# Kernel tuning notes

Measured on AMD Instinct MI355X. Metric: run time of the kernel, lower is better.

## Reference

```python
import jax, jax.numpy as jnp
import numpy as np

BITS = 2
ALPHA = 1.47


def lecac_quantize(w, bits=BITS, alpha=ALPHA):
    """2-bit alpha-scaled weight quantization (LECAC-style fake quant).

    Per-tensor scale derived from mean |w|, scaled by alpha. For bits=2 the
    integer codes live in [-2, 1] (i.e. [-2^(b-1), 2^(b-1)-1]).
    Straight-through estimator: gradient flows as identity through the
    round/clip (stop_gradient trick).
    """
    qmin = -(2 ** (bits - 1))          # -2
    qmax = 2 ** (bits - 1) - 1         # +1
    scale = alpha * jnp.mean(jnp.abs(w)) + jnp.asarray(1e-8, w.dtype)
    q = jnp.clip(jnp.round(w / scale), qmin, qmax)
    w_q = scale * q
    # STE: forward uses w_q, backward passes grad straight through to w
    return w + jax.lax.stop_gradient(w_q - w)


def lecac_linear(x, w, b):
    return jnp.dot(x, lecac_quantize(w).T) + b


def setup_inputs() -> dict:
    key = jax.random.key(0)
    kx, kw1, kb1, kw2, kb2 = jax.random.split(key, 5)
    B, D_IN, D_HID = 262144, 256, 512
    x = jax.random.normal(kx, (B, D_IN), dtype=jnp.float32)
    # Kaiming-ish init like nn.Linear
    W1 = jax.random.normal(kw1, (D_HID, D_IN), dtype=jnp.float32) * (1.0 / np.sqrt(D_IN))
    b1 = jax.random.normal(kb1, (D_HID,), dtype=jnp.float32) * 0.01
    W2 = jax.random.normal(kw2, (D_IN, D_HID), dtype=jnp.float32) * (1.0 / np.sqrt(D_HID))
    b2 = jax.random.normal(kb2, (D_IN,), dtype=jnp.float32) * 0.01
    return {"x": x, "W1": W1, "b1": b1, "W2": W2, "b2": b2}


def reference(x, W1, b1, W2, b2):
    h = jax.nn.relu(lecac_linear(x, W1, b1))   # [B, 512]
    return lecac_linear(h, W2, b2)             # [B, 256]
```

## Files before the change

### kernel.cpp

```cpp
#include <hip/hip_runtime.h>
#include <hip/hip_bf16.h>


typedef __attribute__((ext_vector_type(8))) short bf16x8;
typedef __attribute__((ext_vector_type(4))) float f32x4;
typedef __attribute__((ext_vector_type(4))) unsigned short us4;

#define D_IN 256
#define D_HID 512
#define D_OUT 256
#define BM 32

__device__ __forceinline__ unsigned short f2bf(float f) {
  union { __hip_bfloat16 h; unsigned short u; } c;
  c.h = __float2bfloat16(f);
  return c.u;
}

__device__ __forceinline__ bf16x8 cvt8(float4 lo, float4 hi) {
  bf16x8 v;
  v[0] = (short)f2bf(lo.x); v[1] = (short)f2bf(lo.y);
  v[2] = (short)f2bf(lo.z); v[3] = (short)f2bf(lo.w);
  v[4] = (short)f2bf(hi.x); v[5] = (short)f2bf(hi.y);
  v[6] = (short)f2bf(hi.z); v[7] = (short)f2bf(hi.w);
  return v;
}

__device__ __forceinline__ bf16x8 unpack8(unsigned w, int kkl) {
  unsigned te = (w >> (4 * kkl)) & 0x03030303u;
  unsigned to = (w >> (4 * kkl + 2)) & 0x03030303u;
  int4 o;
  unsigned s;
  s = __builtin_amdgcn_perm(to, te, 0x04040000u) + 0x00040004u;
  o.x = (int)__builtin_amdgcn_perm(0x80008000u, 0xBFC03F00u, s);
  s = __builtin_amdgcn_perm(to, te, 0x05050101u) + 0x00040004u;
  o.y = (int)__builtin_amdgcn_perm(0x80008000u, 0xBFC03F00u, s);
  s = __builtin_amdgcn_perm(to, te, 0x06060202u) + 0x00040004u;
  o.z = (int)__builtin_amdgcn_perm(0x80008000u, 0xBFC03F00u, s);
  s = __builtin_amdgcn_perm(to, te, 0x07070303u) + 0x00040004u;
  o.w = (int)__builtin_amdgcn_perm(0x80008000u, 0xBFC03F00u, s);
  return *(bf16x8*)&o;
}

__global__ void partial_abs_kernel(const float* __restrict__ W1,
                                   const float* __restrict__ W2,
                                   double* __restrict__ part) {
  const int b = blockIdx.x;
  const float* W = (b < 8) ? W1 : W2;
  const float* p = W + (b & 7) * 16384;
  double s = 0.0;
  for (int i = threadIdx.x; i < 16384; i += 1024) s += (double)fabsf(p[i]);
  __shared__ double red[1024];
  red[threadIdx.x] = s;
  __syncthreads();
  for (int st = 512; st > 0; st >>= 1) {
    if (threadIdx.x < st) red[threadIdx.x] += red[threadIdx.x + st];
    __syncthreads();
  }
  if (threadIdx.x == 0) part[b] = red[0];
}

__global__ void pack_kernel(const float* __restrict__ W1,
                            const float* __restrict__ W2,
                            const double* __restrict__ part,
                            unsigned* __restrict__ pk,
                            float* __restrict__ fscales) {
  int idx = blockIdx.x * 1024 + threadIdx.x;
  const double* q = part;
  double sA = 1.47 * ((((q[0]+q[1])+(q[2]+q[3]))+((q[4]+q[5])+(q[6]+q[7]))) / 131072.0) + 1e-8;
  double sB = 1.47 * ((((q[8]+q[9])+(q[10]+q[11]))+((q[12]+q[13])+(q[14]+q[15]))) / 131072.0) + 1e-8;
  if (idx == 0) { fscales[0] = (float)sA; fscales[1] = (float)sB; }
  bool is2 = idx >= 8192;
  int r = idx & 8191;
  int tt = r >> 4;
  int w = r & 15;
  int wv = tt >> 6, lane = tt & 63;
  int l15 = lane & 15, g = (lane >> 4) & 3;
  unsigned word = 0;
  for (int c = 0; c < 4; ++c) {
    for (int b = 0; b < 4; ++b) {
      int j = 2 * b + (c & 1), kkl = c >> 1;
      int code;
      if (!is2) {
        int mf = w >> 2, kp = w & 3;
        int row = 64 * wv + 16 * mf + l15;
        int k = (2 * kp + kkl) * 32 + 8 * g + j;
        double v = rint((double)W1[row * 256 + k] / sA);
        code = (int)fmin(fmax(v, -2.0), 1.0) & 3;
      } else {
        int mf = w >> 3, kp = w & 7;
        int row = 32 * wv + 16 * mf + l15;
        int k = (2 * kp + kkl) * 32 + 8 * g + j;
        double v = rint((double)W2[row * 512 + k] / sB);
        code = (int)fmin(fmax(v, -2.0), 1.0) & 3;
      }
      word |= (unsigned)code << (8 * b + 2 * c);
    }
  }
  pk[idx] = word;
}

__launch_bounds__(512)
__global__ void fused_mlp(const float* __restrict__ x,
                          const float* __restrict__ b1,
                          const float* __restrict__ b2,
                          const unsigned* __restrict__ pk,
                          const float* __restrict__ fscales,
                          float* __restrict__ out) {
  __shared__ unsigned short xs[BM * D_IN];
  __shared__ unsigned short hs[BM * D_HID];
  const int t = threadIdx.x;
  const int lane = t & 63;
  const int wv = t >> 6;
  const int l15 = lane & 15;
  const int g = lane >> 4;
  const long row0 = (long)blockIdx.x * BM;
  const float s1 = fscales[0];
  const float s2 = fscales[1];
  const f32x4 zero4 = {0.f, 0.f, 0.f, 0.f};

  unsigned w1k[16], w2k[16];
  {
    const uint4* p1 = (const uint4*)pk + t * 4;
    const uint4* p2 = (const uint4*)pk + 2048 + t * 4;
#pragma unroll
    for (int i = 0; i < 4; ++i) {
      uint4 a = p1[i], b = p2[i];
      w1k[4*i] = a.x; w1k[4*i+1] = a.y; w1k[4*i+2] = a.z; w1k[4*i+3] = a.w;
      w2k[4*i] = b.x; w2k[4*i+1] = b.y; w2k[4*i+2] = b.z; w2k[4*i+3] = b.w;
    }
  }

  {
    const float4* p = (const float4*)x + (long)blockIdx.x * 2048 + (t >> 4) * 64 + (t & 15) * 4;
    float4 v0 = p[0], v1 = p[1], v2 = p[2], v3 = p[3];
    int r = t >> 4, cq = t & 15;
    bf16x8 e0 = cvt8(v0, v1);
    bf16x8 e1 = cvt8(v2, v3);
    int sw = (r & 7) << 2;
    *(bf16x8*)&xs[r * 256 + ((cq * 2) ^ sw) * 8] = e0;
    *(bf16x8*)&xs[r * 256 + ((cq * 2 + 1) ^ sw) * 8] = e1;
  }
  __syncthreads();

  f32x4 acc1[4][2];
#pragma unroll
  for (int a = 0; a < 4; ++a) { acc1[a][0] = zero4; acc1[a][1] = zero4; }
#pragma unroll
  for (int kp = 0; kp < 4; ++kp) {
#pragma unroll
    for (int kkl = 0; kkl < 2; ++kkl) {
      int kk = 2 * kp + kkl;
      bf16x8 bx[2];
#pragma unroll
      for (int nf = 0; nf < 2; ++nf) {
        int m = 16 * nf + l15;
        int s = (kk * 4 + g) ^ ((m & 7) << 2);
        bx[nf] = *(const bf16x8*)&xs[m * 256 + s * 8];
      }
#pragma unroll
      for (int mf = 0; mf < 4; ++mf) {
        bf16x8 fr = unpack8(w1k[mf * 4 + kp], kkl);
        acc1[mf][0] = __builtin_amdgcn_mfma_f32_16x16x32_bf16(fr, bx[0], acc1[mf][0], 0, 0, 0);
        acc1[mf][1] = __builtin_amdgcn_mfma_f32_16x16x32_bf16(fr, bx[1], acc1[mf][1], 0, 0, 0);
      }
    }
  }

#pragma unroll
  for (int mf = 0; mf < 4; ++mf) {
    int cb = 64 * wv + 16 * mf + 4 * g;
    float4 bb = *(const float4*)&b1[cb];
    int chunk = 8 * wv + 2 * mf + (g >> 1);
    int half = (g & 1) * 4;
#pragma unroll
    for (int nf = 0; nf < 2; ++nf) {
      int m = 16 * nf + l15;
      f32x4 a = acc1[mf][nf];
      us4 o;
      o.x = f2bf(fmaxf(s1 * a[0] + bb.x, 0.f));
      o.y = f2bf(fmaxf(s1 * a[1] + bb.y, 0.f));
      o.z = f2bf(fmaxf(s1 * a[2] + bb.z, 0.f));
      o.w = f2bf(fmaxf(s1 * a[3] + bb.w, 0.f));
      int slot = chunk ^ ((m & 7) << 2);
      *(us4*)&hs[m * D_HID + slot * 8 + half] = o;
    }
  }
  __syncthreads();

  f32x4 acc2[2][2];
#pragma unroll
  for (int a = 0; a < 2; ++a) { acc2[a][0] = zero4; acc2[a][1] = zero4; }
#pragma unroll
  for (int kp = 0; kp < 8; ++kp) {
#pragma unroll
    for (int kkl = 0; kkl < 2; ++kkl) {
      int kk = 2 * kp + kkl;
      bf16x8 bh[2];
#pragma unroll
      for (int nf = 0; nf < 2; ++nf) {
        int m = 16 * nf + l15;
        int s = (kk * 4 + g) ^ ((m & 7) << 2);
        bh[nf] = *(const bf16x8*)&hs[m * D_HID + s * 8];
      }
#pragma unroll
      for (int mf = 0; mf < 2; ++mf) {
        bf16x8 fr = unpack8(w2k[mf * 8 + kp], kkl);
        acc2[mf][0] = __builtin_amdgcn_mfma_f32_16x16x32_bf16(fr, bh[0], acc2[mf][0], 0, 0, 0);
        acc2[mf][1] = __builtin_amdgcn_mfma_f32_16x16x32_bf16(fr, bh[1], acc2[mf][1], 0, 0, 0);
      }
    }
  }

#pragma unroll
  for (int mf = 0; mf < 2; ++mf) {
    int n4 = 32 * wv + 16 * mf + 4 * g;
    float4 bb = *(const float4*)&b2[n4];
#pragma unroll
    for (int nf = 0; nf < 2; ++nf) {
      int m = 16 * nf + l15;
      f32x4 a = acc2[mf][nf];
      float4 o;
      o.x = s2 * a[0] + bb.x;
      o.y = s2 * a[1] + bb.y;
      o.z = s2 * a[2] + bb.z;
      o.w = s2 * a[3] + bb.w;
      *(float4*)&out[(row0 + m) * D_OUT + n4] = o;
    }
  }
}

extern "C" void kernel_launch(void* const* d_in, const int* in_sizes, int n_in,
                              void* d_out, int out_size, void* d_ws, size_t ws_size,
                              hipStream_t stream) {
  const float* x  = (const float*)d_in[0];
  const float* W1 = (const float*)d_in[1];
  const float* b1 = (const float*)d_in[2];
  const float* W2 = (const float*)d_in[3];
  const float* b2 = (const float*)d_in[4];
  float* out = (float*)d_out;

  double* part = (double*)d_ws;
  float* fsc = (float*)((char*)d_ws + 128);
  unsigned* pk = (unsigned*)((char*)d_ws + 1024);

  int Brows = in_sizes[0] / D_IN;
  int nblk = Brows / BM;

  partial_abs_kernel<<<dim3(16), dim3(1024), 0, stream>>>(W1, W2, part);
  pack_kernel<<<dim3(16), dim3(1024), 0, stream>>>(W1, W2, part, pk, fsc);
  fused_mlp<<<dim3(nblk), dim3(512), 0, stream>>>(x, b1, b2, pk, fsc, out);
}
```

Before: 220.1 us.

## Persistent 1024-thread blocks over 4 row tiles with double-buffered x prefetch

```diff
diff --git a/kernel.cpp b/kernel.cpp
--- a/kernel.cpp
+++ b/kernel.cpp
@@ -9,7 +9,8 @@
 #define D_IN 256
 #define D_HID 512
 #define D_OUT 256
-#define BM 32
+#define BM 64
+#define TILES 4
 
 __device__ __forceinline__ unsigned short f2bf(float f) {
   union { __hip_bfloat16 h; unsigned short u; } c;
@@ -72,8 +73,8 @@
   if (idx == 0) { fscales[0] = (float)sA; fscales[1] = (float)sB; }
   bool is2 = idx >= 8192;
   int r = idx & 8191;
-  int tt = r >> 4;
-  int w = r & 15;
+  int tt = r >> 3;
+  int w = r & 7;
   int wv = tt >> 6, lane = tt & 63;
   int l15 = lane & 15, g = (lane >> 4) & 3;
   unsigned word = 0;
@@ -83,13 +84,13 @@
       int code;
       if (!is2) {
         int mf = w >> 2, kp = w & 3;
-        int row = 64 * wv + 16 * mf + l15;
+        int row = 32 * wv + 16 * mf + l15;
         int k = (2 * kp + kkl) * 32 + 8 * g + j;
         double v = rint((double)W1[row * 256 + k] / sA);
         code = (int)fmin(fmax(v, -2.0), 1.0) & 3;
       } else {
-        int mf = w >> 3, kp = w & 7;
-        int row = 32 * wv + 16 * mf + l15;
+        int kp = w;
+        int row = 16 * wv + l15;
         int k = (2 * kp + kkl) * 32 + 8 * g + j;
         double v = rint((double)W2[row * 512 + k] / sB);
         code = (int)fmin(fmax(v, -2.0), 1.0) & 3;
@@ -100,133 +101,157 @@
   pk[idx] = word;
 }
 
-__launch_bounds__(512)
+__launch_bounds__(1024)
 __global__ void fused_mlp(const float* __restrict__ x,
                           const float* __restrict__ b1,
                           const float* __restrict__ b2,
                           const unsigned* __restrict__ pk,
                           const float* __restrict__ fscales,
                           float* __restrict__ out) {
-  __shared__ unsigned short xs[BM * D_IN];
+  __shared__ unsigned short xs[2][BM * D_IN];
   __shared__ unsigned short hs[BM * D_HID];
   const int t = threadIdx.x;
   const int lane = t & 63;
   const int wv = t >> 6;
   const int l15 = lane & 15;
   const int g = lane >> 4;
-  const long row0 = (long)blockIdx.x * BM;
+  const long tbase = (long)blockIdx.x * TILES;
   const float s1 = fscales[0];
   const float s2 = fscales[1];
   const f32x4 zero4 = {0.f, 0.f, 0.f, 0.f};
 
-  unsigned w1k[16], w2k[16];
+  unsigned w1k[8], w2k[8];
   {
-    const uint4* p1 = (const uint4*)pk + t * 4;
-    const uint4* p2 = (const uint4*)pk + 2048 + t * 4;
-#pragma unroll
-    for (int i = 0; i < 4; ++i) {
+    const uint4* p1 = (const uint4*)pk + t * 2;
+    const uint4* p2 = (const uint4*)(pk + 8192) + t * 2;
+#pragma unroll
+    for (int i = 0; i < 2; ++i) {
       uint4 a = p1[i], b = p2[i];
       w1k[4*i] = a.x; w1k[4*i+1] = a.y; w1k[4*i+2] = a.z; w1k[4*i+3] = a.w;
       w2k[4*i] = b.x; w2k[4*i+1] = b.y; w2k[4*i+2] = b.z; w2k[4*i+3] = b.w;
     }
   }
 
-  {
-    const float4* p = (const float4*)x + (long)blockIdx.x * 2048 + (t >> 4) * 64 + (t & 15) * 4;
-    float4 v0 = p[0], v1 = p[1], v2 = p[2], v3 = p[3];
-    int r = t >> 4, cq = t & 15;
-    bf16x8 e0 = cvt8(v0, v1);
-    bf16x8 e1 = cvt8(v2, v3);
-    int sw = (r & 7) << 2;
-    *(bf16x8*)&xs[r * 256 + ((cq * 2) ^ sw) * 8] = e0;
-    *(bf16x8*)&xs[r * 256 + ((cq * 2 + 1) ^ sw) * 8] = e1;
-  }
-  __syncthreads();
-
-  f32x4 acc1[4][2];
-#pragma unroll
-  for (int a = 0; a < 4; ++a) { acc1[a][0] = zero4; acc1[a][1] = zero4; }
-#pragma unroll
-  for (int kp = 0; kp < 4; ++kp) {
-#pragma unroll
-    for (int kkl = 0; kkl < 2; ++kkl) {
-      int kk = 2 * kp + kkl;
-      bf16x8 bx[2];
-#pragma unroll
-      for (int nf = 0; nf < 2; ++nf) {
+  float4 xv[4];
+
+  auto loadxv = [&](long tile) {
+    const float4* p = (const float4*)x + tile * 4096;
+    xv[0] = p[2 * t];
+    xv[1] = p[2 * t + 1];
+    xv[2] = p[2048 + 2 * t];
+    xv[3] = p[2049 + 2 * t];
+  };
+  auto stagex = [&](int buf) {
+    unsigned short* xb = xs[buf];
+    int m0 = t >> 5;
+    int sl0 = (t & 31);
+    bf16x8 e0 = cvt8(xv[0], xv[1]);
+    *(bf16x8*)&xb[m0 * 256 + (sl0 ^ ((m0 & 7) << 2)) * 8] = e0;
+    int m1 = 32 + m0;
+    bf16x8 e1 = cvt8(xv[2], xv[3]);
+    *(bf16x8*)&xb[m1 * 256 + (sl0 ^ ((m1 & 7) << 2)) * 8] = e1;
+  };
+
+  f32x4 acc1[2][4];
+  f32x4 acc2[4];
+
+  loadxv(tbase);
+  stagex(0);
+  loadxv(tbase + 1);
+  asm volatile("s_waitcnt lgkmcnt(0)" ::: "memory");
+  __builtin_amdgcn_s_barrier();
+
+  for (int i = 0; i < TILES; ++i) {
+    const unsigned short* xb = xs[i & 1];
+#pragma unroll
+    for (int a = 0; a < 2; ++a)
+#pragma unroll
+      for (int b = 0; b < 4; ++b) acc1[a][b] = zero4;
+#pragma unroll
+    for (int kp = 0; kp < 4; ++kp) {
+#pragma unroll
+      for (int kkl = 0; kkl < 2; ++kkl) {
+        int kk = 2 * kp + kkl;
+        bf16x8 bx[4];
+#pragma unroll
+        for (int nf = 0; nf < 4; ++nf) {
+          int m = 16 * nf + l15;
+          int s = (kk * 4 + g) ^ ((m & 7) << 2);
+          bx[nf] = *(const bf16x8*)&xb[m * 256 + s * 8];
+        }
+#pragma unroll
+        for (int mf = 0; mf < 2; ++mf) {
+          bf16x8 fr = unpack8(w1k[mf * 4 + kp], kkl);
+#pragma unroll
+          for (int nf = 0; nf < 4; ++nf)
+            acc1[mf][nf] = __builtin_amdgcn_mfma_f32_16x16x32_bf16(fr, bx[nf], acc1[mf][nf], 0, 0, 0);
+        }
+      }
+    }
+
+#pragma unroll
+    for (int mf = 0; mf < 2; ++mf) {
+      int cb = 32 * wv + 16 * mf + 4 * g;
+      float4 bb = *(const float4*)&b1[cb];
+      int chunk = 4 * wv + 2 * mf + (g >> 1);
+      int half = (g & 1) * 4;
+#pragma unroll
+      for (int nf = 0; nf < 4; ++nf) {
         int m = 16 * nf + l15;
-        int s = (kk * 4 + g) ^ ((m & 7) << 2);
-        bx[nf] = *(const bf16x8*)&xs[m * 256 + s * 8];
-      }
-#pragma unroll
-      for (int mf = 0; mf < 4; ++mf) {
-        bf16x8 fr = unpack8(w1k[mf * 4 + kp], kkl);
-        acc1[mf][0] = __builtin_amdgcn_mfma_f32_16x16x32_bf16(fr, bx[0], acc1[mf][0], 0, 0, 0);
-        acc1[mf][1] = __builtin_amdgcn_mfma_f32_16x16x32_bf16(fr, bx[1], acc1[mf][1], 0, 0, 0);
-      }
-    }
-  }
-
-#pragma unroll
-  for (int mf = 0; mf < 4; ++mf) {
-    int cb = 64 * wv + 16 * mf + 4 * g;
-    float4 bb = *(const float4*)&b1[cb];
-    int chunk = 8 * wv + 2 * mf + (g >> 1);
-    int half = (g & 1) * 4;
-#pragma unroll
-    for (int nf = 0; nf < 2; ++nf) {
-      int m = 16 * nf + l15;
-      f32x4 a = acc1[mf][nf];
-      us4 o;
-      o.x = f2bf(fmaxf(s1 * a[0] + bb.x, 0.f));
-      o.y = f2bf(fmaxf(s1 * a[1] + bb.y, 0.f));
-      o.z = f2bf(fmaxf(s1 * a[2] + bb.z, 0.f));
-      o.w = f2bf(fmaxf(s1 * a[3] + bb.w, 0.f));
-      int slot = chunk ^ ((m & 7) << 2);
-      *(us4*)&hs[m * D_HID + slot * 8 + half] = o;
-    }
-  }
-  __syncthreads();
-
-  f32x4 acc2[2][2];
-#pragma unroll
-  for (int a = 0; a < 2; ++a) { acc2[a][0] = zero4; acc2[a][1] = zero4; }
-#pragma unroll
-  for (int kp = 0; kp < 8; ++kp) {
-#pragma unroll
-    for (int kkl = 0; kkl < 2; ++kkl) {
-      int kk = 2 * kp + kkl;
-      bf16x8 bh[2];
-#pragma unroll
-      for (int nf = 0; nf < 2; ++nf) {
+        f32x4 a = acc1[mf][nf];
+        us4 o;
+        o.x = f2bf(fmaxf(s1 * a[0] + bb.x, 0.f));
+        o.y = f2bf(fmaxf(s1 * a[1] + bb.y, 0.f));
+        o.z = f2bf(fmaxf(s1 * a[2] + bb.z, 0.f));
+        o.w = f2bf(fmaxf(s1 * a[3] + bb.w, 0.f));
+        int slot = chunk ^ ((m & 7) << 2);
+        *(us4*)&hs[m * D_HID + slot * 8 + half] = o;
+      }
+    }
+    if (i + 1 < TILES) stagex((i + 1) & 1);
+    if (i + 2 < TILES) loadxv(tbase + i + 2);
+    asm volatile("s_waitcnt lgkmcnt(0)" ::: "memory");
+    __builtin_amdgcn_s_barrier();
+
+#pragma unroll
+    for (int b = 0; b < 4; ++b) acc2[b] = zero4;
+#pragma unroll
+    for (int kp = 0; kp < 8; ++kp) {
+#pragma unroll
+      for (int kkl = 0; kkl < 2; ++kkl) {
+        int kk = 2 * kp + kkl;
+        bf16x8 bh[4];
+#pragma unroll
+        for (int nf = 0; nf < 4; ++nf) {
+          int m = 16 * nf + l15;
+          int s = (kk * 4 + g) ^ ((m & 7) << 2);
+          bh[nf] = *(const bf16x8*)&hs[m * D_HID + s * 8];
+        }
+        bf16x8 fr = unpack8(w2k[kp], kkl);
+#pragma unroll
+        for (int nf = 0; nf < 4; ++nf)
+          acc2[nf] = __builtin_amdgcn_mfma_f32_16x16x32_bf16(fr, bh[nf], acc2[nf], 0, 0, 0);
+      }
+    }
+
+    {
+      const long row0 = (tbase + i) * BM;
+      int n4 = 16 * wv + 4 * g;
+      float4 bb = *(const float4*)&b2[n4];
+#pragma unroll
+      for (int nf = 0; nf < 4; ++nf) {
         int m = 16 * nf + l15;
-        int s = (kk * 4 + g) ^ ((m & 7) << 2);
-        bh[nf] = *(const bf16x8*)&hs[m * D_HID + s * 8];
-      }
-#pragma unroll
-      for (int mf = 0; mf < 2; ++mf) {
-        bf16x8 fr = unpack8(w2k[mf * 8 + kp], kkl);
-        acc2[mf][0] = __builtin_amdgcn_mfma_f32_16x16x32_bf16(fr, bh[0], acc2[mf][0], 0, 0, 0);
-        acc2[mf][1] = __builtin_amdgcn_mfma_f32_16x16x32_bf16(fr, bh[1], acc2[mf][1], 0, 0, 0);
-      }
-    }
-  }
-
-#pragma unroll
-  for (int mf = 0; mf < 2; ++mf) {
-    int n4 = 32 * wv + 16 * mf + 4 * g;
-    float4 bb = *(const float4*)&b2[n4];
-#pragma unroll
-    for (int nf = 0; nf < 2; ++nf) {
-      int m = 16 * nf + l15;
-      f32x4 a = acc2[mf][nf];
-      float4 o;
-      o.x = s2 * a[0] + bb.x;
-      o.y = s2 * a[1] + bb.y;
-      o.z = s2 * a[2] + bb.z;
-      o.w = s2 * a[3] + bb.w;
-      *(float4*)&out[(row0 + m) * D_OUT + n4] = o;
-    }
+        f32x4 a = acc2[nf];
+        float4 o;
+        o.x = s2 * a[0] + bb.x;
+        o.y = s2 * a[1] + bb.y;
+        o.z = s2 * a[2] + bb.z;
+        o.w = s2 * a[3] + bb.w;
+        *(float4*)&out[(row0 + m) * D_OUT + n4] = o;
+      }
+    }
+    asm volatile("s_waitcnt lgkmcnt(0)" ::: "memory");
+    __builtin_amdgcn_s_barrier();
   }
 }
 
@@ -245,9 +270,9 @@
   unsigned* pk = (unsigned*)((char*)d_ws + 1024);
 
   int Brows = in_sizes[0] / D_IN;
-  int nblk = Brows / BM;
+  int nblk = Brows / (BM * TILES);
 
   partial_abs_kernel<<<dim3(16), dim3(1024), 0, stream>>>(W1, W2, part);
   pack_kernel<<<dim3(16), dim3(1024), 0, stream>>>(W1, W2, part, pk, fsc);
-  fused_mlp<<<dim3(nblk), dim3(512), 0, stream>>>(x, b1, b2, pk, fsc, out);
-}
+  fused_mlp<<<dim3(nblk), dim3(1024), 0, stream>>>(x, b1, b2, pk, fsc, out);
+}
```

Result: slower. 506.8 us (+130.3%).

## Make fused MLP persistent over 8 row tiles with double-buffered x prefetch

Applied to the files above, without the earlier changes.

```diff
diff --git a/kernel.cpp b/kernel.cpp
--- a/kernel.cpp
+++ b/kernel.cpp
@@ -10,6 +10,7 @@
 #define D_HID 512
 #define D_OUT 256
 #define BM 32
+#define TILES 8
 
 __device__ __forceinline__ unsigned short f2bf(float f) {
   union { __hip_bfloat16 h; unsigned short u; } c;
@@ -107,14 +108,14 @@
                           const unsigned* __restrict__ pk,
                           const float* __restrict__ fscales,
                           float* __restrict__ out) {
-  __shared__ unsigned short xs[BM * D_IN];
+  __shared__ unsigned short xs[2][BM * D_IN];
   __shared__ unsigned short hs[BM * D_HID];
   const int t = threadIdx.x;
   const int lane = t & 63;
   const int wv = t >> 6;
   const int l15 = lane & 15;
   const int g = lane >> 4;
-  const long row0 = (long)blockIdx.x * BM;
+  const long tbase = (long)blockIdx.x * TILES;
   const float s1 = fscales[0];
   const float s2 = fscales[1];
   const f32x4 zero4 = {0.f, 0.f, 0.f, 0.f};
@@ -131,102 +132,121 @@
     }
   }
 
-  {
-    const float4* p = (const float4*)x + (long)blockIdx.x * 2048 + (t >> 4) * 64 + (t & 15) * 4;
-    float4 v0 = p[0], v1 = p[1], v2 = p[2], v3 = p[3];
-    int r = t >> 4, cq = t & 15;
-    bf16x8 e0 = cvt8(v0, v1);
-    bf16x8 e1 = cvt8(v2, v3);
-    int sw = (r & 7) << 2;
-    *(bf16x8*)&xs[r * 256 + ((cq * 2) ^ sw) * 8] = e0;
-    *(bf16x8*)&xs[r * 256 + ((cq * 2 + 1) ^ sw) * 8] = e1;
-  }
-  __syncthreads();
+  float4 xv[4];
+  auto loadx = [&](long tile) {
+    const float4* p = (const float4*)x + tile * 2048 + (t >> 4) * 64 + (t & 15) * 4;
+    xv[0] = p[0]; xv[1] = p[1]; xv[2] = p[2]; xv[3] = p[3];
+  };
+  auto writex = [&](int buf) {
+    int r = t >> 4, cq = t & 15, sw = (r & 7) << 2;
+    bf16x8 e0 = cvt8(xv[0], xv[1]);
+    bf16x8 e1 = cvt8(xv[2], xv[3]);
+    *(bf16x8*)&xs[buf][r * 256 + ((cq * 2) ^ sw) * 8] = e0;
+    *(bf16x8*)&xs[buf][r * 256 + ((cq * 2 + 1) ^ sw) * 8] = e1;
+  };
 
   f32x4 acc1[4][2];
-#pragma unroll
-  for (int a = 0; a < 4; ++a) { acc1[a][0] = zero4; acc1[a][1] = zero4; }
-#pragma unroll
-  for (int kp = 0; kp < 4; ++kp) {
-#pragma unroll
-    for (int kkl = 0; kkl < 2; ++kkl) {
-      int kk = 2 * kp + kkl;
-      bf16x8 bx[2];
+  f32x4 acc2[2][2];
+
+  loadx(tbase);
+  writex(0);
+  asm volatile("s_waitcnt lgkmcnt(0)" ::: "memory");
+  __builtin_amdgcn_s_barrier();
+
+  for (int i = 0; i < TILES; ++i) {
+    const unsigned short* xb = xs[i & 1];
+#pragma unroll
+    for (int a = 0; a < 4; ++a) { acc1[a][0] = zero4; acc1[a][1] = zero4; }
+#pragma unroll
+    for (int kp = 0; kp < 4; ++kp) {
+#pragma unroll
+      for (int kkl = 0; kkl < 2; ++kkl) {
+        int kk = 2 * kp + kkl;
+        bf16x8 bx[2];
+#pragma unroll
+        for (int nf = 0; nf < 2; ++nf) {
+          int m = 16 * nf + l15;
+          int s = (kk * 4 + g) ^ ((m & 7) << 2);
+          bx[nf] = *(const bf16x8*)&xb[m * 256 + s * 8];
+        }
+#pragma unroll
+        for (int mf = 0; mf < 4; ++mf) {
+          bf16x8 fr = unpack8(w1k[mf * 4 + kp], kkl);
+          acc1[mf][0] = __builtin_amdgcn_mfma_f32_16x16x32_bf16(fr, bx[0], acc1[mf][0], 0, 0, 0);
+          acc1[mf][1] = __builtin_amdgcn_mfma_f32_16x16x32_bf16(fr, bx[1], acc1[mf][1], 0, 0, 0);
+        }
+      }
+    }
+
+    if (i + 1 < TILES) loadx(tbase + i + 1);
+
+#pragma unroll
+    for (int mf = 0; mf < 4; ++mf) {
+      int cb = 64 * wv + 16 * mf + 4 * g;
+      float4 bb = *(const float4*)&b1[cb];
+      int chunk = 8 * wv + 2 * mf + (g >> 1);
+      int half = (g & 1) * 4;
 #pragma unroll
       for (int nf = 0; nf < 2; ++nf) {
         int m = 16 * nf + l15;
-        int s = (kk * 4 + g) ^ ((m & 7) << 2);
-        bx[nf] = *(const bf16x8*)&xs[m * 256 + s * 8];
-      }
-#pragma unroll
-      for (int mf = 0; mf < 4; ++mf) {
-        bf16x8 fr = unpack8(w1k[mf * 4 + kp], kkl);
-        acc1[mf][0] = __builtin_amdgcn_mfma_f32_16x16x32_bf16(fr, bx[0], acc1[mf][0], 0, 0, 0);
-        acc1[mf][1] = __builtin_amdgcn_mfma_f32_16x16x32_bf16(fr, bx[1], acc1[mf][1], 0, 0, 0);
-      }
-    }
-  }
-
-#pragma unroll
-  for (int mf = 0; mf < 4; ++mf) {
-    int cb = 64 * wv + 16 * mf + 4 * g;
-    float4 bb = *(const float4*)&b1[cb];
-    int chunk = 8 * wv + 2 * mf + (g >> 1);
-    int half = (g & 1) * 4;
-#pragma unroll
-    for (int nf = 0; nf < 2; ++nf) {
-      int m = 16 * nf + l15;
-      f32x4 a = acc1[mf][nf];
-      us4 o;
-      o.x = f2bf(fmaxf(s1 * a[0] + bb.x, 0.f));
-      o.y = f2bf(fmaxf(s1 * a[1] + bb.y, 0.f));
-      o.z = f2bf(fmaxf(s1 * a[2] + bb.z, 0.f));
-      o.w = f2bf(fmaxf(s1 * a[3] + bb.w, 0.f));
-      int slot = chunk ^ ((m & 7) << 2);
-      *(us4*)&hs[m * D_HID + slot * 8 + half] = o;
-    }
-  }
-  __syncthreads();
-
-  f32x4 acc2[2][2];
-#pragma unroll
-  for (int a = 0; a < 2; ++a) { acc2[a][0] = zero4; acc2[a][1] = zero4; }
-#pragma unroll
-  for (int kp = 0; kp < 8; ++kp) {
-#pragma unroll
-    for (int kkl = 0; kkl < 2; ++kkl) {
-      int kk = 2 * kp + kkl;
-      bf16x8 bh[2];
-#pragma unroll
-      for (int nf = 0; nf < 2; ++nf) {
-        int m = 16 * nf + l15;
-        int s = (kk * 4 + g) ^ ((m & 7) << 2);
-        bh[nf] = *(const bf16x8*)&hs[m * D_HID + s * 8];
-      }
+        f32x4 a = acc1[mf][nf];
+        us4 o;
+        o.x = f2bf(fmaxf(s1 * a[0] + bb.x, 0.f));
+        o.y = f2bf(fmaxf(s1 * a[1] + bb.y, 0.f));
+        o.z = f2bf(fmaxf(s1 * a[2] + bb.z, 0.f));
+        o.w = f2bf(fmaxf(s1 * a[3] + bb.w, 0.f));
+        int slot = chunk ^ ((m & 7) << 2);
+        *(us4*)&hs[m * D_HID + slot * 8 + half] = o;
+      }
+    }
+    if (i + 1 < TILES) writex((i + 1) & 1);
+    asm volatile("s_waitcnt lgkmcnt(0)" ::: "memory");
+    __builtin_amdgcn_s_barrier();
+
+#pragma unroll
+    for (int a = 0; a < 2; ++a) { acc2[a][0] = zero4; acc2[a][1] = zero4; }
+#pragma unroll
+    for (int kp = 0; kp < 8; ++kp) {
+#pragma unroll
+      for (int kkl = 0; kkl < 2; ++kkl) {
+        int kk = 2 * kp + kkl;
+        bf16x8 bh[2];
+#pragma unroll
+        for (int nf = 0; nf < 2; ++nf) {
+          int m = 16 * nf + l15;
+          int s = (kk * 4 + g) ^ ((m & 7) << 2);
+          bh[nf] = *(const bf16x8*)&hs[m * D_HID + s * 8];
+        }
+#pragma unroll
+        for (int mf = 0; mf < 2; ++mf) {
+          bf16x8 fr = unpack8(w2k[mf * 8 + kp], kkl);
+          acc2[mf][0] = __builtin_amdgcn_mfma_f32_16x16x32_bf16(fr, bh[0], acc2[mf][0], 0, 0, 0);
+          acc2[mf][1] = __builtin_amdgcn_mfma_f32_16x16x32_bf16(fr, bh[1], acc2[mf][1], 0, 0, 0);
+        }
+      }
+    }
+
+    {
+      const long row0 = (tbase + i) * BM;
 #pragma unroll
       for (int mf = 0; mf < 2; ++mf) {
-        bf16x8 fr = unpack8(w2k[mf * 8 + kp], kkl);
-        acc2[mf][0] = __builtin_amdgcn_mfma_f32_16x16x32_bf16(fr, bh[0], acc2[mf][0], 0, 0, 0);
-        acc2[mf][1] = __builtin_amdgcn_mfma_f32_16x16x32_bf16(fr, bh[1], acc2[mf][1], 0, 0, 0);
-      }
-    }
-  }
-
-#pragma unroll
-  for (int mf = 0; mf < 2; ++mf) {
-    int n4 = 32 * wv + 16 * mf + 4 * g;
-    float4 bb = *(const float4*)&b2[n4];
-#pragma unroll
-    for (int nf = 0; nf < 2; ++nf) {
-      int m = 16 * nf + l15;
-      f32x4 a = acc2[mf][nf];
-      float4 o;
-      o.x = s2 * a[0] + bb.x;
-      o.y = s2 * a[1] + bb.y;
-      o.z = s2 * a[2] + bb.z;
-      o.w = s2 * a[3] + bb.w;
-      *(float4*)&out[(row0 + m) * D_OUT + n4] = o;
-    }
+        int n4 = 32 * wv + 16 * mf + 4 * g;
+        float4 bb = *(const float4*)&b2[n4];
+#pragma unroll
+        for (int nf = 0; nf < 2; ++nf) {
+          int m = 16 * nf + l15;
+          f32x4 a = acc2[mf][nf];
+          float4 o;
+          o.x = s2 * a[0] + bb.x;
+          o.y = s2 * a[1] + bb.y;
+          o.z = s2 * a[2] + bb.z;
+          o.w = s2 * a[3] + bb.w;
+          *(float4*)&out[(row0 + m) * D_OUT + n4] = o;
+        }
+      }
+    }
+    asm volatile("s_waitcnt lgkmcnt(0)" ::: "memory");
+    __builtin_amdgcn_s_barrier();
   }
 }
 
@@ -245,7 +265,7 @@
   unsigned* pk = (unsigned*)((char*)d_ws + 1024);
 
   int Brows = in_sizes[0] / D_IN;
-  int nblk = Brows / BM;
+  int nblk = Brows / (BM * TILES);
 
   partial_abs_kernel<<<dim3(16), dim3(1024), 0, stream>>>(W1, W2, part);
   pack_kernel<<<dim3(16), dim3(1024), 0, stream>>>(W1, W2, part, pk, fsc);
```

After: 481.5 us. 2.19x slower.
